# Kernel optimization log

Measured on AMD Instinct MI355X. Metric: run time of the kernel, lower is better.

The kernel has to match this reference:

```python
import math
import jax, jax.numpy as jnp
import numpy as np

D_MODEL = 1024
NUM_HEADS = 16
D_K = D_MODEL // NUM_HEADS
THETA = 10000.0
MAX_SEQ_LEN = 2048
BATCH = 2
SEQ = 2048


def build_rope_matrices(theta, d_k, max_seq_len):
    # Faithful to the torch buffer: per-position d_k x d_k tridiagonal rotation matrix.
    k = jnp.arange(d_k)
    inv_freq = jnp.power(theta, -2.0 * (k // 2) / d_k)  # [d_k]
    pos = jnp.arange(max_seq_len, dtype=jnp.float32)[:, None]  # [S,1]
    ang = pos * inv_freq[None, :]  # [S, d_k]
    cos_v = jnp.cos(ang)  # main diagonal
    sin_v = jnp.sin(jnp.where(k % 2 == 0, ang, 0.0))[:, :-1]  # sub/super diagonal, len d_k-1

    def mk(c, s):
        return jnp.diag(c) + jnp.diag(s, -1) + jnp.diag(-s, 1)

    return jax.vmap(mk)(cos_v, sin_v)  # [max_seq_len, d_k, d_k]


def setup_inputs() -> dict:
    key = jax.random.key(0)
    k1, k2, k3 = jax.random.split(key, 3)
    x = jax.random.normal(k1, (BATCH, SEQ, D_MODEL), dtype=jnp.float32)
    token_positions = jnp.arange(SEQ, dtype=jnp.int64 if jax.config.jax_enable_x64 else jnp.int32)
    # trunc_normal init approximated by scaled normal (same distribution family / scale)
    std_attn = 2.0 / (D_MODEL + 3 * D_MODEL)
    std_out = 2.0 / (D_MODEL + D_MODEL)
    W_attn = jax.random.normal(k2, (3 * NUM_HEADS * D_K, D_MODEL), dtype=jnp.float32) * std_attn
    W_out = jax.random.normal(k3, (D_MODEL, NUM_HEADS * D_K), dtype=jnp.float32) * std_out
    rope = build_rope_matrices(THETA, D_K, MAX_SEQ_LEN)
    return {"x": x, "W_attn": W_attn, "W_out": W_out, "rope": rope,
            "token_positions": token_positions}


def reference(x, W_attn, W_out, rope, token_positions):
    B, S, _ = x.shape
    # QKV projection: '... d_in, d_out d_in -> ... d_out'
    proj = jnp.einsum('bsd,ed->bse', x, W_attn)  # [B,S,3*H*dk]
    proj = proj.reshape(B, S, 3, NUM_HEADS, D_K)
    proj = jnp.transpose(proj, (2, 0, 3, 1, 4))  # [3,B,H,S,dk]
    Q, K, V = proj[0], proj[1], proj[2]
    # RoPE via per-position matrix multiply (faithful to module)
    R = rope[token_positions]  # [S, dk, dk]
    Q = jnp.einsum('sij,bhsj->bhsi', R, Q)
    K = jnp.einsum('sij,bhsj->bhsi', R, K)
    # naive causal attention with full score matrix (faithful)
    scores = jnp.einsum('bhnd,bhmd->bhnm', Q, K) / math.sqrt(D_K)
    causal = jnp.tril(jnp.ones((S, S), dtype=bool))
    scores = jnp.where(causal, scores, -jnp.inf)
    attn = jax.nn.softmax(scores, axis=-1)
    attended = jnp.einsum('bhnm,bhmd->bhnd', attn, V)  # [B,H,S,dk]
    concat = jnp.transpose(attended, (0, 2, 1, 3)).reshape(B, S, NUM_HEADS * D_K)
    return jnp.einsum('bse,de->bsd', concat, W_out)
```

## Files before the change

### kernel.cpp

```cpp
#include <hip/hip_runtime.h>
#include <math.h>

#define B_SZ 2
#define SEQ 2048
#define DMODEL 1024
#define NH 16
#define DK 64
#define NQKV 3072
#define M_ROWS 4096

#define NEG_BIG (-3.0e38f)
#define SCL 0.18033688011112042f

typedef short short8 __attribute__((ext_vector_type(8)));
typedef float v4f __attribute__((ext_vector_type(4)));
typedef unsigned short ushort_t;

__device__ inline ushort_t f2bf(float f) {
    unsigned u = __float_as_uint(f);
    u += 0x7fffu + ((u >> 16) & 1u);
    return (ushort_t)(u >> 16);
}

__device__ __forceinline__ unsigned cvt_pk_bf16(float lo, float hi) {
    unsigned r;
    asm("v_cvt_pk_bf16_f32 %0, %1, %2" : "=v"(r) : "v"(lo), "v"(hi));
    return r;
}
__device__ __forceinline__ void permlane32_swap(unsigned &a, unsigned &b) {
    asm("v_permlane32_swap_b32 %0, %1" : "+v"(a), "+v"(b));
}
__device__ __forceinline__ void permlane16_swap(unsigned &a, unsigned &b) {
    asm("v_permlane16_swap_b32 %0, %1" : "+v"(a), "+v"(b));
}

__device__ __forceinline__ void gl_lds16(const ushort_t* g, ushort_t* l) {
    __builtin_amdgcn_global_load_lds(
        (const __attribute__((address_space(1))) unsigned int*)g,
        (__attribute__((address_space(3))) unsigned int*)l, 16, 0, 0);
}

__device__ __forceinline__ int kvaddr(int row, int col8) {
    return row * 64 + ((col8 ^ (row & 7)) << 3);
}

__global__ __launch_bounds__(256) void prep_kernel(
    const float* __restrict__ x, const float* __restrict__ Wa,
    const float* __restrict__ Wo, const float* __restrict__ rope,
    ushort_t* __restrict__ xb, ushort_t* __restrict__ Wab, ushort_t* __restrict__ Wob,
    float* __restrict__ cosT, float* __restrict__ sinT)
{
    (void)rope;
    const int bid = blockIdx.x;
    if (bid < 8192) {
        const float* src; ushort_t* dst; int i;
        if (bid < 4096)      { src = x;  dst = xb;  i = bid * 256 + threadIdx.x; }
        else if (bid < 7168) { src = Wa; dst = Wab; i = (bid - 4096) * 256 + threadIdx.x; }
        else                 { src = Wo; dst = Wob; i = (bid - 7168) * 256 + threadIdx.x; }
        float4 v = reinterpret_cast<const float4*>(src)[i];
        ushort4 r;
        r.x = f2bf(v.x); r.y = f2bf(v.y); r.z = f2bf(v.z); r.w = f2bf(v.w);
        reinterpret_cast<ushort4*>(dst)[i] = r;
    } else {
        const int i = (bid - 8192) * 256 + threadIdx.x;
        const int p = i >> 6, d = i & 63;
        const float inv = exp2f(-0.4152410118609203f * (float)(d >> 1));
        const float ang = (float)p * inv;
        float sv, cv;
        sincosf(ang, &sv, &cv);
        cosT[i] = cv;
        sinT[i] = (d & 1) ? sv : -sv;
    }
}

#define ES_STRIDE 136

#define QKV_STAGE(bofs, k0s)                                                   \
    _Pragma("unroll")                                                          \
    for (int j = 0; j < 4; ++j)                                                \
        gl_lds16(&Wab[(size_t)(e0 + srow[j]) * DMODEL + (k0s) + skc[j]],       \
                 &qkv_smem[(bofs) + (tid + 256 * j) * 8]);                     \
    _Pragma("unroll")                                                          \
    for (int j = 4; j < 8; ++j)                                                \
        gl_lds16(&xb[(size_t)(m0 + srow[j]) * DMODEL + (k0s) + skc[j]],        \
                 &qkv_smem[(bofs) + (tid + 256 * j) * 8]);

__global__ __launch_bounds__(256) void qkv_mfma_kernel(
    const ushort_t* __restrict__ xb,
    const ushort_t* __restrict__ Wab,
    const float* __restrict__ cosT, const float* __restrict__ sinT,
    const int* __restrict__ tpos,
    ushort_t* __restrict__ Qb, ushort_t* __restrict__ Kb, ushort_t* __restrict__ Vtb)
{
    __shared__ ushort_t qkv_smem[32768];
    ushort_t* Es = qkv_smem;

    const int tid = threadIdx.x;
    const int w = tid >> 6, lane = tid & 63;
    const int lm = lane & 15, g = lane >> 4;
    const int wm = (w >> 1) * 64, wn = (w & 1) * 64;

    const int lid = blockIdx.y * 24 + blockIdx.x;
    const int swz = (lid & 7) * 96 + (lid >> 3);
    const int e0 = (swz % 24) * 128, m0 = (swz / 24) * 128;

    int srow[8], skc[8];
#pragma unroll
    for (int j = 0; j < 8; ++j) {
        const int c = tid + 256 * j;
        const int cm = c & 1023;
        const int row = cm >> 3, pp = cm & 7;
        srow[j] = row;
        skc[j] = (pp ^ (row & 7)) * 8;
    }

    v4f acc[4][4] = {};

    QKV_STAGE(0, 0);

    for (int t = 0; t < 16; ++t) {
        const int bofs = (t & 1) << 14;
        if (t < 15) {
            const int nofs = ((t + 1) & 1) << 14;
            QKV_STAGE(nofs, (t + 1) * 64);
            __builtin_amdgcn_sched_barrier(0);
            asm volatile("s_waitcnt vmcnt(8)" ::: "memory");
        } else {
            __builtin_amdgcn_sched_barrier(0);
            asm volatile("s_waitcnt vmcnt(0)" ::: "memory");
        }
        __builtin_amdgcn_s_barrier();
        __builtin_amdgcn_sched_barrier(0);

        __builtin_amdgcn_s_setprio(1);
#pragma unroll
        for (int kb = 0; kb < 2; ++kb) {
            short8 af[4], bfr[4];
#pragma unroll
            for (int mf = 0; mf < 4; ++mf) {
                const int r = wm + mf * 16 + lm;
                af[mf] = *reinterpret_cast<const short8*>(
                    &qkv_smem[bofs + (r * 8 + ((kb * 4 + g) ^ (r & 7))) * 8]);
            }
#pragma unroll
            for (int nf = 0; nf < 4; ++nf) {
                const int r = wn + nf * 16 + lm;
                bfr[nf] = *reinterpret_cast<const short8*>(
                    &qkv_smem[bofs + 8192 + (r * 8 + ((kb * 4 + g) ^ (r & 7))) * 8]);
            }
#pragma unroll
            for (int mf = 0; mf < 4; ++mf)
#pragma unroll
                for (int nf = 0; nf < 4; ++nf)
                    acc[mf][nf] = __builtin_amdgcn_mfma_f32_16x16x32_bf16(af[mf], bfr[nf], acc[mf][nf], 0, 0, 0);
        }
        __builtin_amdgcn_s_setprio(0);

        __builtin_amdgcn_sched_barrier(0);
        __builtin_amdgcn_s_barrier();
        __builtin_amdgcn_sched_barrier(0);
    }

    __syncthreads();

    const int which = e0 >> 10;
    const int h0 = (e0 & 1023) >> 6;
    const int bb = m0 >> 11, s0 = m0 & 2047;

    if (which < 2) {
        ushort_t* buf = (which == 0) ? Qb : Kb;
        const float qs = (which == 0) ? SCL : 1.0f;
#pragma unroll
        for (int mf = 0; mf < 4; ++mf) {
            const int ebase = wm + mf * 16 + g * 4;
            const int d0 = (e0 + ebase) & 63;
#pragma unroll
            for (int nf = 0; nf < 4; ++nf) {
                const int sloc = wn + nf * 16 + lm;
                float v[4] = {acc[mf][nf][0], acc[mf][nf][1], acc[mf][nf][2], acc[mf][nf][3]};
                const int p = tpos[s0 + sloc];
                const float4 c4 = *reinterpret_cast<const float4*>(&cosT[p * 64 + d0]);
                const float4 s4 = *reinterpret_cast<const float4*>(&sinT[p * 64 + d0]);
                const float r0 = (c4.x * v[0] + s4.x * v[1]) * qs;
                const float r1 = (c4.y * v[1] + s4.y * v[0]) * qs;
                const float r2 = (c4.z * v[2] + s4.z * v[3]) * qs;
                const float r3 = (c4.w * v[3] + s4.w * v[2]) * qs;
                uint2 pp;
                pp.x = (unsigned)f2bf(r0) | ((unsigned)f2bf(r1) << 16);
                pp.y = (unsigned)f2bf(r2) | ((unsigned)f2bf(r3) << 16);
                *reinterpret_cast<uint2*>(&Es[sloc * ES_STRIDE + ebase]) = pp;
            }
        }
        __syncthreads();
#pragma unroll
        for (int hh = 0; hh < 2; ++hh) {
            ushort_t* dst = buf + (((size_t)bb * NH + h0 + hh) * SEQ + s0) * DK;
#pragma unroll
            for (int t = 0; t < 4; ++t) {
                const int o = (t * 256 + tid) * 8;
                const int sloc = o >> 6, d = o & 63;
                const short8 vv = *reinterpret_cast<const short8*>(&Es[sloc * ES_STRIDE + hh * 64 + d]);
                *reinterpret_cast<short8*>(&dst[o]) = vv;
            }
        }
    } else {
#pragma unroll
        for (int mf = 0; mf < 4; ++mf) {
            const int ebase = wm + mf * 16 + g * 4;
#pragma unroll
            for (int nf = 0; nf < 4; ++nf) {
                const int sloc = wn + nf * 16 + lm;
                Es[(ebase + 0) * ES_STRIDE + sloc] = f2bf(acc[mf][nf][0]);
                Es[(ebase + 1) * ES_STRIDE + sloc] = f2bf(acc[mf][nf][1]);
                Es[(ebase + 2) * ES_STRIDE + sloc] = f2bf(acc[mf][nf][2]);
                Es[(ebase + 3) * ES_STRIDE + sloc] = f2bf(acc[mf][nf][3]);
            }
        }
        __syncthreads();
#pragma unroll
        for (int t = 0; t < 8; ++t) {
            const int c = t * 256 + tid;
            const int hh = c >> 10, cm = c & 1023;
            const int d = cm >> 4, s8c = (cm & 15) * 8;
            const short8 vv = *reinterpret_cast<const short8*>(&Es[(hh * 64 + d) * ES_STRIDE + s8c]);
            ushort_t* dst = Vtb + ((size_t)bb * NH + h0 + hh) * SEQ * DK + (size_t)d * SEQ + s0 + s8c;
            *reinterpret_cast<short8*>(dst) = vv;
        }
    }
}

#define ATTN_STEP(QF0, QF1, QROW, LACC, OACC, DIAG, C0)                           \
    {                                                                             \
        v4f sacc[4] = {};                                                         \
        _Pragma("unroll")                                                         \
        for (int nf = 0; nf < 4; ++nf) {                                          \
            sacc[nf] = __builtin_amdgcn_mfma_f32_16x16x32_bf16(kf[nf][0], QF0, sacc[nf], 0, 0, 0); \
            sacc[nf] = __builtin_amdgcn_mfma_f32_16x16x32_bf16(kf[nf][1], QF1, sacc[nf], 0, 0, 0); \
        }                                                                         \
        if (DIAG) {                                                               \
            _Pragma("unroll")                                                     \
            for (int nf = 0; nf < 4; ++nf)                                        \
                _Pragma("unroll")                                                 \
                for (int reg = 0; reg < 4; ++reg) {                               \
                    const int kv = (C0) + nf * 16 + g * 4 + reg;                  \
                    if (kv > (QROW)) sacc[nf][reg] = NEG_BIG;                     \
                }                                                                 \
        }                                                                         \
        unsigned pk0[8];                                                          \
        _Pragma("unroll")                                                         \
        for (int nf = 0; nf < 4; ++nf) {                                          \
            pk0[nf * 2]     = cvt_pk_bf16(exp2f(sacc[nf][0]), exp2f(sacc[nf][1])); \
            pk0[nf * 2 + 1] = cvt_pk_bf16(exp2f(sacc[nf][2]), exp2f(sacc[nf][3])); \
        }                                                                         \
        _Pragma("unroll")                                                         \
        for (int kc = 0; kc < 2; ++kc) {                                          \
            unsigned x0 = pk0[kc * 4 + 0], y0 = pk0[kc * 4 + 2];                  \
            unsigned x1 = pk0[kc * 4 + 1], y1 = pk0[kc * 4 + 3];                  \
            permlane32_swap(x0, y0); permlane16_swap(x0, y0);                     \
            permlane32_swap(x1, y1); permlane16_swap(x1, y1);                     \
            union { unsigned u[4]; short8 s; } pu;                                \
            pu.u[0] = x0; pu.u[1] = x1; pu.u[2] = y0; pu.u[3] = y1;               \
            const short8 pf = pu.s;                                               \
            LACC = __builtin_amdgcn_mfma_f32_16x16x32_bf16(ones8, pf, LACC, 0, 0, 0); \
            _Pragma("unroll")                                                     \
            for (int df = 0; df < 4; ++df)                                        \
                OACC[df] = __builtin_amdgcn_mfma_f32_16x16x32_bf16(vf[df][kc], pf, OACC[df], 0, 0, 0); \
        }                                                                         \
    }

__global__ __launch_bounds__(256, 2) void attn_mfma_kernel(
    const ushort_t* __restrict__ Qb, const ushort_t* __restrict__ Kb,
    const ushort_t* __restrict__ Vtb, ushort_t* __restrict__ attb)
{
    __shared__ ushort_t Ks[2][4096];
    __shared__ ushort_t Vs[2][4096];

    const int tid = threadIdx.x;
    const int w = tid >> 6, lane = tid & 63;
    const int lm = lane & 15, g = lane >> 4, lk8 = g * 8;

    const int u = blockIdx.x;
    const int h = blockIdx.y, b = blockIdx.z;
    const size_t ho = ((size_t)b * NH + h) * SEQ * DK;
    const ushort_t* Qh = Qb + ho;
    const ushort_t* Kh = Kb + ho;
    const ushort_t* Vth = Vtb + ho;

    const int rr0 = tid >> 3, c80 = tid & 7;
    const int rr1 = rr0 + 32, c81 = c80;
    const int sw0 = kvaddr(rr0, c80);
    const int sw1 = kvaddr(rr1, c81);
    const int gc0 = c80 * 8, gc1 = c81 * 8;

    const int it1 = u, it2 = 31 - u;
    const int qrowA = it1 * 64 + w * 16 + lm;
    const int qrowB = it2 * 64 + w * 16 + lm;

    const short8 qa0 = *reinterpret_cast<const short8*>(&Qh[(size_t)qrowA * DK + lk8]);
    const short8 qa1 = *reinterpret_cast<const short8*>(&Qh[(size_t)qrowA * DK + 32 + lk8]);
    const short8 qb0 = *reinterpret_cast<const short8*>(&Qh[(size_t)qrowB * DK + lk8]);
    const short8 qb1 = *reinterpret_cast<const short8*>(&Qh[(size_t)qrowB * DK + 32 + lk8]);

    const short8 ones8 = {16256, 16256, 16256, 16256, 16256, 16256, 16256, 16256};

    v4f laccA = {}, laccB = {};
    v4f OA[4] = {}, OB[4] = {};

    short8 kreg[2], vreg[2];
    kreg[0] = *reinterpret_cast<const short8*>(&Kh[(size_t)rr0 * DK + gc0]);
    kreg[1] = *reinterpret_cast<const short8*>(&Kh[(size_t)rr1 * DK + gc1]);
    vreg[0] = *reinterpret_cast<const short8*>(&Vth[(size_t)rr0 * SEQ + gc0]);
    vreg[1] = *reinterpret_cast<const short8*>(&Vth[(size_t)rr1 * SEQ + gc1]);

    for (int jt = 0; jt <= it2; ++jt) {
        const int c0 = jt * 64;
        const int bufi = jt & 1;
        ushort_t* Ksb = Ks[bufi];
        ushort_t* Vsb = Vs[bufi];

        *reinterpret_cast<short8*>(&Ksb[sw0]) = kreg[0];
        *reinterpret_cast<short8*>(&Ksb[sw1]) = kreg[1];
        *reinterpret_cast<short8*>(&Vsb[sw0]) = vreg[0];
        *reinterpret_cast<short8*>(&Vsb[sw1]) = vreg[1];

        if (jt < it2) {
            const int c0n = c0 + 64;
            kreg[0] = *reinterpret_cast<const short8*>(&Kh[(size_t)(c0n + rr0) * DK + gc0]);
            kreg[1] = *reinterpret_cast<const short8*>(&Kh[(size_t)(c0n + rr1) * DK + gc1]);
            vreg[0] = *reinterpret_cast<const short8*>(&Vth[(size_t)rr0 * SEQ + c0n + gc0]);
            vreg[1] = *reinterpret_cast<const short8*>(&Vth[(size_t)rr1 * SEQ + c0n + gc1]);
        }

        __syncthreads();

        short8 kf[4][2], vf[4][2];
#pragma unroll
        for (int nf = 0; nf < 4; ++nf) {
            const int r = nf * 16 + lm;
            kf[nf][0] = *reinterpret_cast<const short8*>(&Ksb[kvaddr(r, g)]);
            kf[nf][1] = *reinterpret_cast<const short8*>(&Ksb[kvaddr(r, 4 + g)]);
        }
#pragma unroll
        for (int df = 0; df < 4; ++df) {
            const int r = df * 16 + lm;
            vf[df][0] = *reinterpret_cast<const short8*>(&Vsb[kvaddr(r, g)]);
            vf[df][1] = *reinterpret_cast<const short8*>(&Vsb[kvaddr(r, 4 + g)]);
        }

        ATTN_STEP(qb0, qb1, qrowB, laccB, OB, (jt == it2), c0)
        if (jt <= it1) {
            ATTN_STEP(qa0, qa1, qrowA, laccA, OA, (jt == it1), c0)
        }
    }

    {
        const float inv = 1.0f / laccA[0];
#pragma unroll
        for (int df = 0; df < 4; ++df) {
            uint2 st;
            st.x = cvt_pk_bf16(OA[df][0] * inv, OA[df][1] * inv);
            st.y = cvt_pk_bf16(OA[df][2] * inv, OA[df][3] * inv);
            *reinterpret_cast<uint2*>(
                &attb[((size_t)b * SEQ + qrowA) * DMODEL + h * DK + df * 16 + g * 4]) = st;
        }
    }
    {
        const float inv = 1.0f / laccB[0];
#pragma unroll
        for (int df = 0; df < 4; ++df) {
            uint2 st;
            st.x = cvt_pk_bf16(OB[df][0] * inv, OB[df][1] * inv);
            st.y = cvt_pk_bf16(OB[df][2] * inv, OB[df][3] * inv);
            *reinterpret_cast<uint2*>(
                &attb[((size_t)b * SEQ + qrowB) * DMODEL + h * DK + df * 16 + g * 4]) = st;
        }
    }
}

#define OUT_STAGE(bofs, k0s)                                                   \
    _Pragma("unroll")                                                          \
    for (int j = 0; j < 4; ++j)                                                \
        gl_lds16(&attb[(size_t)(m0 + srow[j]) * DMODEL + (k0s) + skc[j]],      \
                 &smem[(bofs) + (tid + 256 * j) * 8]);                         \
    _Pragma("unroll")                                                          \
    for (int j = 4; j < 8; ++j)                                                \
        gl_lds16(&Wob[(size_t)(n0 + srow[j]) * DMODEL + (k0s) + skc[j]],       \
                 &smem[(bofs) + (tid + 256 * j) * 8]);

__global__ __launch_bounds__(256) void out_mfma_kernel(
    const ushort_t* __restrict__ attb,
    const ushort_t* __restrict__ Wob,
    float* __restrict__ out)
{
    __shared__ ushort_t smem[32768];

    const int tid = threadIdx.x;
    const int w = tid >> 6, lane = tid & 63;
    const int lm = lane & 15, g = lane >> 4;
    const int wm = (w >> 1) * 64, wn = (w & 1) * 64;

    const int lid = blockIdx.y * 8 + blockIdx.x;
    const int swz = (lid & 7) * 32 + (lid >> 3);
    const int m0 = (swz >> 3) * 128, n0 = (swz & 7) * 128;

    int srow[8], skc[8];
#pragma unroll
    for (int j = 0; j < 8; ++j) {
        const int c = tid + 256 * j;
        const int cm = c & 1023;
        const int row = cm >> 3, pp = cm & 7;
        srow[j] = row;
        skc[j] = (pp ^ (row & 7)) * 8;
    }

    v4f acc[4][4] = {};

    OUT_STAGE(0, 0);

    for (int t = 0; t < 16; ++t) {
        const int bofs = (t & 1) << 14;
        if (t < 15) {
            const int nofs = ((t + 1) & 1) << 14;
            OUT_STAGE(nofs, (t + 1) * 64);
            __builtin_amdgcn_sched_barrier(0);
            asm volatile("s_waitcnt vmcnt(8)" ::: "memory");
        } else {
            __builtin_amdgcn_sched_barrier(0);
            asm volatile("s_waitcnt vmcnt(0)" ::: "memory");
        }
        __builtin_amdgcn_s_barrier();
        __builtin_amdgcn_sched_barrier(0);

        __builtin_amdgcn_s_setprio(1);
#pragma unroll
        for (int kb = 0; kb < 2; ++kb) {
            short8 af[4], bfr[4];
#pragma unroll
            for (int mf = 0; mf < 4; ++mf) {
                const int r = wm + mf * 16 + lm;
                af[mf] = *reinterpret_cast<const short8*>(
                    &smem[bofs + (r * 8 + ((kb * 4 + g) ^ (r & 7))) * 8]);
            }
#pragma unroll
            for (int nf = 0; nf < 4; ++nf) {
                const int r = wn + nf * 16 + lm;
                bfr[nf] = *reinterpret_cast<const short8*>(
                    &smem[bofs + 8192 + (r * 8 + ((kb * 4 + g) ^ (r & 7))) * 8]);
            }
#pragma unroll
            for (int mf = 0; mf < 4; ++mf)
#pragma unroll
                for (int nf = 0; nf < 4; ++nf)
                    acc[mf][nf] = __builtin_amdgcn_mfma_f32_16x16x32_bf16(af[mf], bfr[nf], acc[mf][nf], 0, 0, 0);
        }
        __builtin_amdgcn_s_setprio(0);

        __builtin_amdgcn_sched_barrier(0);
        __builtin_amdgcn_s_barrier();
        __builtin_amdgcn_sched_barrier(0);
    }

#pragma unroll
    for (int mf = 0; mf < 4; ++mf)
#pragma unroll
        for (int reg = 0; reg < 4; ++reg) {
            const int m = m0 + wm + mf * 16 + g * 4 + reg;
#pragma unroll
            for (int nf = 0; nf < 4; ++nf) {
                const int n = n0 + wn + nf * 16 + lm;
                out[(size_t)m * DMODEL + n] = acc[mf][nf][reg];
            }
        }
}

extern "C" void kernel_launch(void* const* d_in, const int* in_sizes, int n_in,
                              void* d_out, int out_size, void* d_ws, size_t ws_size,
                              hipStream_t stream) {
    (void)in_sizes; (void)n_in; (void)out_size; (void)ws_size;

    const float* x    = (const float*)d_in[0];
    const float* Wa   = (const float*)d_in[1];
    const float* Wo   = (const float*)d_in[2];
    const float* rope = (const float*)d_in[3];
    const int*   tp   = (const int*)d_in[4];
    float* out = (float*)d_out;

    char* ws = (char*)d_ws;
    ushort_t* xb   = (ushort_t*)(ws);
    ushort_t* Wab  = (ushort_t*)(ws + (8u << 20));
    ushort_t* Wob  = (ushort_t*)(ws + (14u << 20));
    float*    cosT = (float*)   (ws + (16u << 20));
    float*    sinT = (float*)   (ws + (16u << 20) + (512u << 10));
    ushort_t* Qb   = (ushort_t*)(ws + (17u << 20));
    ushort_t* Kb   = (ushort_t*)(ws + (25u << 20));
    ushort_t* Vtb  = (ushort_t*)(ws + (33u << 20));
    ushort_t* attb = (ushort_t*)(ws + (41u << 20));

    dim3 blk(256);
    prep_kernel<<<dim3(8704), blk, 0, stream>>>(x, Wa, Wo, rope, xb, Wab, Wob, cosT, sinT);

    qkv_mfma_kernel<<<dim3(NQKV / 128, M_ROWS / 128), blk, 0, stream>>>(
        xb, Wab, cosT, sinT, tp, Qb, Kb, Vtb);
    attn_mfma_kernel<<<dim3(16, NH, B_SZ), blk, 0, stream>>>(Qb, Kb, Vtb, attb);
    out_mfma_kernel<<<dim3(DMODEL / 128, M_ROWS / 128), blk, 0, stream>>>(attb, Wob, out);
}
```

Measured before the change: 196.5 us.

## Prefetch K/V two tiles ahead in attention; halve out-proj N tile

The attention loop is manually unrolled by two, with separate register sets for even and odd K/V tiles. This lets global loads be issued two tiles ahead, hiding more memory latency at the cost of extra registers. Separately, the output projection GEMM now uses 128x64 tiles instead of 128x128, doubling the grid to 512 blocks to improve CU occupancy. That shrinks shared memory and accumulators per block but reduces data reuse.

```diff
diff --git a/kernel.cpp b/kernel.cpp
--- a/kernel.cpp
+++ b/kernel.cpp
@@ -268,6 +268,42 @@
         }                                                                         \
     }
 
+#define ATTN_ITER(JT, KR0, KR1, VR0, VR1)                                         \
+    {                                                                             \
+        const int c0 = (JT) * 64;                                                 \
+        ushort_t* Ksb = Ks[(JT) & 1];                                             \
+        ushort_t* Vsb = Vs[(JT) & 1];                                             \
+        *reinterpret_cast<short8*>(&Ksb[sw0]) = KR0;                              \
+        *reinterpret_cast<short8*>(&Ksb[sw1]) = KR1;                              \
+        *reinterpret_cast<short8*>(&Vsb[sw0]) = VR0;                              \
+        *reinterpret_cast<short8*>(&Vsb[sw1]) = VR1;                              \
+        if ((JT) + 2 <= it2) {                                                    \
+            const int c0n = c0 + 128;                                             \
+            KR0 = *reinterpret_cast<const short8*>(&Kh[(size_t)(c0n + rr0) * DK + gc0]);  \
+            KR1 = *reinterpret_cast<const short8*>(&Kh[(size_t)(c0n + rr1) * DK + gc1]);  \
+            VR0 = *reinterpret_cast<const short8*>(&Vth[(size_t)rr0 * SEQ + c0n + gc0]);  \
+            VR1 = *reinterpret_cast<const short8*>(&Vth[(size_t)rr1 * SEQ + c0n + gc1]);  \
+        }                                                                         \
+        __syncthreads();                                                          \
+        short8 kf[4][2], vf[4][2];                                                \
+        _Pragma("unroll")                                                         \
+        for (int nf = 0; nf < 4; ++nf) {                                          \
+            const int r = nf * 16 + lm;                                           \
+            kf[nf][0] = *reinterpret_cast<const short8*>(&Ksb[kvaddr(r, g)]);     \
+            kf[nf][1] = *reinterpret_cast<const short8*>(&Ksb[kvaddr(r, 4 + g)]); \
+        }                                                                         \
+        _Pragma("unroll")                                                         \
+        for (int df = 0; df < 4; ++df) {                                          \
+            const int r = df * 16 + lm;                                           \
+            vf[df][0] = *reinterpret_cast<const short8*>(&Vsb[kvaddr(r, g)]);     \
+            vf[df][1] = *reinterpret_cast<const short8*>(&Vsb[kvaddr(r, 4 + g)]); \
+        }                                                                         \
+        ATTN_STEP(qb0, qb1, qrowB, laccB, OB, ((JT) == it2), c0)                  \
+        if ((JT) <= it1) {                                                        \
+            ATTN_STEP(qa0, qa1, qrowA, laccA, OA, ((JT) == it1), c0)              \
+        }                                                                         \
+    }
+
 __global__ __launch_bounds__(256, 2) void attn_mfma_kernel(
     const ushort_t* __restrict__ Qb, const ushort_t* __restrict__ Kb,
     const ushort_t* __restrict__ Vtb, ushort_t* __restrict__ attb)
@@ -306,50 +342,19 @@
     v4f laccA = {}, laccB = {};
     v4f OA[4] = {}, OB[4] = {};
 
-    short8 kreg[2], vreg[2];
-    kreg[0] = *reinterpret_cast<const short8*>(&Kh[(size_t)rr0 * DK + gc0]);
-    kreg[1] = *reinterpret_cast<const short8*>(&Kh[(size_t)rr1 * DK + gc1]);
-    vreg[0] = *reinterpret_cast<const short8*>(&Vth[(size_t)rr0 * SEQ + gc0]);
-    vreg[1] = *reinterpret_cast<const short8*>(&Vth[(size_t)rr1 * SEQ + gc1]);
-
-    for (int jt = 0; jt <= it2; ++jt) {
-        const int c0 = jt * 64;
-        const int bufi = jt & 1;
-        ushort_t* Ksb = Ks[bufi];
-        ushort_t* Vsb = Vs[bufi];
-
-        *reinterpret_cast<short8*>(&Ksb[sw0]) = kreg[0];
-        *reinterpret_cast<short8*>(&Ksb[sw1]) = kreg[1];
-        *reinterpret_cast<short8*>(&Vsb[sw0]) = vreg[0];
-        *reinterpret_cast<short8*>(&Vsb[sw1]) = vreg[1];
-
-        if (jt < it2) {
-            const int c0n = c0 + 64;
-            kreg[0] = *reinterpret_cast<const short8*>(&Kh[(size_t)(c0n + rr0) * DK + gc0]);
-            kreg[1] = *reinterpret_cast<const short8*>(&Kh[(size_t)(c0n + rr1) * DK + gc1]);
-            vreg[0] = *reinterpret_cast<const short8*>(&Vth[(size_t)rr0 * SEQ + c0n + gc0]);
-            vreg[1] = *reinterpret_cast<const short8*>(&Vth[(size_t)rr1 * SEQ + c0n + gc1]);
-        }
-
-        __syncthreads();
-
-        short8 kf[4][2], vf[4][2];
-#pragma unroll
-        for (int nf = 0; nf < 4; ++nf) {
-            const int r = nf * 16 + lm;
-            kf[nf][0] = *reinterpret_cast<const short8*>(&Ksb[kvaddr(r, g)]);
-            kf[nf][1] = *reinterpret_cast<const short8*>(&Ksb[kvaddr(r, 4 + g)]);
-        }
-#pragma unroll
-        for (int df = 0; df < 4; ++df) {
-            const int r = df * 16 + lm;
-            vf[df][0] = *reinterpret_cast<const short8*>(&Vsb[kvaddr(r, g)]);
-            vf[df][1] = *reinterpret_cast<const short8*>(&Vsb[kvaddr(r, 4 + g)]);
-        }
-
-        ATTN_STEP(qb0, qb1, qrowB, laccB, OB, (jt == it2), c0)
-        if (jt <= it1) {
-            ATTN_STEP(qa0, qa1, qrowA, laccA, OA, (jt == it1), c0)
+    short8 kE0 = *reinterpret_cast<const short8*>(&Kh[(size_t)rr0 * DK + gc0]);
+    short8 kE1 = *reinterpret_cast<const short8*>(&Kh[(size_t)rr1 * DK + gc1]);
+    short8 vE0 = *reinterpret_cast<const short8*>(&Vth[(size_t)rr0 * SEQ + gc0]);
+    short8 vE1 = *reinterpret_cast<const short8*>(&Vth[(size_t)rr1 * SEQ + gc1]);
+    short8 kO0 = *reinterpret_cast<const short8*>(&Kh[(size_t)(64 + rr0) * DK + gc0]);
+    short8 kO1 = *reinterpret_cast<const short8*>(&Kh[(size_t)(64 + rr1) * DK + gc1]);
+    short8 vO0 = *reinterpret_cast<const short8*>(&Vth[(size_t)rr0 * SEQ + 64 + gc0]);
+    short8 vO1 = *reinterpret_cast<const short8*>(&Vth[(size_t)rr1 * SEQ + 64 + gc1]);
+
+    for (int jt = 0; jt <= it2; jt += 2) {
+        ATTN_ITER(jt, kE0, kE1, vE0, vE1)
+        if (jt + 1 <= it2) {
+            ATTN_ITER(jt + 1, kO0, kO1, vO0, vO1)
         }
     }
 
@@ -383,7 +388,7 @@
         gl_lds16(&attb[(size_t)(m0 + srow[j]) * DMODEL + (k0s) + skc[j]],      \
                  &smem[(bofs) + (tid + 256 * j) * 8]);                         \
     _Pragma("unroll")                                                          \
-    for (int j = 4; j < 8; ++j)                                                \
+    for (int j = 4; j < 6; ++j)                                                \
         gl_lds16(&Wob[(size_t)(n0 + srow[j]) * DMODEL + (k0s) + skc[j]],       \
                  &smem[(bofs) + (tid + 256 * j) * 8]);
 
@@ -392,38 +397,38 @@
     const ushort_t* __restrict__ Wob,
     float* __restrict__ out)
 {
-    __shared__ ushort_t smem[32768];
+    __shared__ ushort_t smem[24576];
 
     const int tid = threadIdx.x;
     const int w = tid >> 6, lane = tid & 63;
     const int lm = lane & 15, g = lane >> 4;
-    const int wm = (w >> 1) * 64, wn = (w & 1) * 64;
-
-    const int lid = blockIdx.y * 8 + blockIdx.x;
-    const int swz = (lid & 7) * 32 + (lid >> 3);
-    const int m0 = (swz >> 3) * 128, n0 = (swz & 7) * 128;
-
-    int srow[8], skc[8];
-#pragma unroll
-    for (int j = 0; j < 8; ++j) {
+    const int wm = (w >> 1) * 64, wn = (w & 1) * 32;
+
+    const int lid = blockIdx.y * 16 + blockIdx.x;
+    const int swz = (lid & 7) * 64 + (lid >> 3);
+    const int m0 = (swz >> 4) * 128, n0 = (swz & 15) * 64;
+
+    int srow[6], skc[6];
+#pragma unroll
+    for (int j = 0; j < 6; ++j) {
         const int c = tid + 256 * j;
-        const int cm = c & 1023;
+        const int cm = (j < 4) ? c : (c - 1024);
         const int row = cm >> 3, pp = cm & 7;
         srow[j] = row;
         skc[j] = (pp ^ (row & 7)) * 8;
     }
 
-    v4f acc[4][4] = {};
+    v4f acc[4][2] = {};
 
     OUT_STAGE(0, 0);
 
     for (int t = 0; t < 16; ++t) {
-        const int bofs = (t & 1) << 14;
+        const int bofs = (t & 1) * 12288;
         if (t < 15) {
-            const int nofs = ((t + 1) & 1) << 14;
+            const int nofs = ((t + 1) & 1) * 12288;
             OUT_STAGE(nofs, (t + 1) * 64);
             __builtin_amdgcn_sched_barrier(0);
-            asm volatile("s_waitcnt vmcnt(8)" ::: "memory");
+            asm volatile("s_waitcnt vmcnt(6)" ::: "memory");
         } else {
             __builtin_amdgcn_sched_barrier(0);
             asm volatile("s_waitcnt vmcnt(0)" ::: "memory");
@@ -434,7 +439,7 @@
         __builtin_amdgcn_s_setprio(1);
 #pragma unroll
         for (int kb = 0; kb < 2; ++kb) {
-            short8 af[4], bfr[4];
+            short8 af[4], bfr[2];
 #pragma unroll
             for (int mf = 0; mf < 4; ++mf) {
                 const int r = wm + mf * 16 + lm;
@@ -442,7 +447,7 @@
                     &smem[bofs + (r * 8 + ((kb * 4 + g) ^ (r & 7))) * 8]);
             }
 #pragma unroll
-            for (int nf = 0; nf < 4; ++nf) {
+            for (int nf = 0; nf < 2; ++nf) {
                 const int r = wn + nf * 16 + lm;
                 bfr[nf] = *reinterpret_cast<const short8*>(
                     &smem[bofs + 8192 + (r * 8 + ((kb * 4 + g) ^ (r & 7))) * 8]);
@@ -450,7 +455,7 @@
 #pragma unroll
             for (int mf = 0; mf < 4; ++mf)
 #pragma unroll
-                for (int nf = 0; nf < 4; ++nf)
+                for (int nf = 0; nf < 2; ++nf)
                     acc[mf][nf] = __builtin_amdgcn_mfma_f32_16x16x32_bf16(af[mf], bfr[nf], acc[mf][nf], 0, 0, 0);
         }
         __builtin_amdgcn_s_setprio(0);
@@ -466,7 +471,7 @@
         for (int reg = 0; reg < 4; ++reg) {
             const int m = m0 + wm + mf * 16 + g * 4 + reg;
 #pragma unroll
-            for (int nf = 0; nf < 4; ++nf) {
+            for (int nf = 0; nf < 2; ++nf) {
                 const int n = n0 + wn + nf * 16 + lm;
                 out[(size_t)m * DMODEL + n] = acc[mf][nf][reg];
             }
@@ -502,5 +507,5 @@
     qkv_mfma_kernel<<<dim3(NQKV / 128, M_ROWS / 128), blk, 0, stream>>>(
         xb, Wab, cosT, sinT, tp, Qb, Kb, Vtb);
     attn_mfma_kernel<<<dim3(16, NH, B_SZ), blk, 0, stream>>>(Qb, Kb, Vtb, attb);
-    out_mfma_kernel<<<dim3(DMODEL / 128, M_ROWS / 128), blk, 0, stream>>>(attb, Wob, out);
-}
+    out_mfma_kernel<<<dim3(16, 32), blk, 0, stream>>>(attb, Wob, out);
+}
```

After: 193.9 us, median of 3. About the same (-1.3%).
